# Performance work log

Measured on AMD Instinct MI355X. Metric: run time of the kernel, lower is better.

The kernel has to match this reference:

```python
import jax, jax.numpy as jnp
import numpy as np

NUM_HEADS = 32
NUM_KV_HEADS = 8
HEAD_DIM = 128
ROPE_THETA = 1000000.0
SCALING = HEAD_DIM ** -0.5


def apply_rope_neox(x, positions):
    # x: [T, H, D], positions: [T] int
    half = HEAD_DIM // 2
    inv_freq = 1.0 / (ROPE_THETA ** (jnp.arange(0, half, dtype=jnp.float32) / half))
    freqs = positions.astype(jnp.float32)[:, None] * inv_freq[None, :]  # [T, D/2]
    cos = jnp.cos(freqs)[:, None, :]  # [T, 1, D/2]
    sin = jnp.sin(freqs)[:, None, :]
    x1, x2 = x[..., :half], x[..., half:]
    return jnp.concatenate([x1 * cos - x2 * sin, x2 * cos + x1 * sin], axis=-1)


def setup_inputs() -> dict:
    key = jax.random.key(0)
    k1, k2, k3 = jax.random.split(key, 3)
    T, H = 2048, 4096
    positions = jnp.arange(T, dtype=jnp.int32)
    hidden_states = jax.random.normal(k1, (T, H), dtype=jnp.float32)
    Wqkv = jax.random.normal(k2, (H, 6144), dtype=jnp.float32) * 0.02
    Wo = jax.random.normal(k3, (H, H), dtype=jnp.float32) * 0.02
    return {"positions": positions, "hidden_states": hidden_states, "Wqkv": Wqkv, "Wo": Wo}


def reference(positions, hidden_states, Wqkv, Wo):
    T = hidden_states.shape[0]
    q_size = NUM_HEADS * HEAD_DIM
    kv_size = NUM_KV_HEADS * HEAD_DIM
    qkv = hidden_states @ Wqkv  # [T, 6144]
    q = qkv[:, :q_size].reshape(T, NUM_HEADS, HEAD_DIM)
    k = qkv[:, q_size:q_size + kv_size].reshape(T, NUM_KV_HEADS, HEAD_DIM)
    v = qkv[:, q_size + kv_size:].reshape(T, NUM_KV_HEADS, HEAD_DIM)
    q = apply_rope_neox(q, positions)
    k = apply_rope_neox(k, positions)
    # GQA: repeat kv heads to match query heads
    rep = NUM_HEADS // NUM_KV_HEADS
    k = jnp.repeat(k, rep, axis=1)  # [T, H, D]
    v = jnp.repeat(v, rep, axis=1)
    scores = jnp.einsum('thd,shd->hts', q, k) * SCALING  # [H, T, T]
    causal = jnp.tril(jnp.ones((T, T), dtype=bool))
    scores = jnp.where(causal[None], scores, jnp.finfo(scores.dtype).min)
    attn = jax.nn.softmax(scores, axis=-1)
    out = jnp.einsum('hts,shd->thd', attn, v).reshape(T, NUM_HEADS * HEAD_DIM)
    return out @ Wo
```

## Files before the change

kernel.cpp:

```cpp
#include <hip/hip_runtime.h>
#include <math.h>

#define T_TOK 2048
#define HDIM  4096
#define QKVN  6144
#define NHEADS 32
#define HD    128
#define KV_OFF 4096
#define V_OFF  5120
#define SCALE 0.08838834764831843f

typedef __attribute__((ext_vector_type(8))) short short8;
typedef __attribute__((ext_vector_type(4))) float f32x4;
typedef __attribute__((ext_vector_type(16))) float f32x16;

__device__ __forceinline__ ushort f2bf(float f) {
    union { float f; unsigned u; } v; v.f = f;
    unsigned r = v.u + 0x7FFFu + ((v.u >> 16) & 1u);
    return (ushort)(r >> 16);
}

template <int N_, int LDK, int KC>
__global__ __launch_bounds__(512, 2) void gemm_bf16_8ph(const ushort* __restrict__ A,
                                                        const ushort* __restrict__ B,
                                                        float* __restrict__ C0,
                                                        float* __restrict__ C1) {
    __shared__ __attribute__((aligned(16))) ushort As[2][2][8192];
    __shared__ __attribute__((aligned(16))) ushort Bs[2][2][8192];

    constexpr int NT = KC / 64;
    constexpr int NBN = N_ / 256;

    const int kz = blockIdx.y;
    float* __restrict__ C = kz ? C1 : C0;

    const int nwgx = (int)gridDim.x;
    const int bid = (int)blockIdx.x;
    const int swz = (nwgx & 7) ? bid : ((bid & 7) * (nwgx >> 3) + (bid >> 3));
    const int bm = (swz / NBN) * 256;
    const int bn = (swz % NBN) * 256;

    const int tid = (int)threadIdx.x;
    const int w = tid >> 6;
    const int l = tid & 63;
    const int hfa = w >> 2;
    const int hfb = (w & 3) >> 1;
    const int wbr64 = (w & 1) * 4096;

    const int arc = (l & 15) * 64;
    const int ac0 = ((((l >> 4) << 4)) ^ ((l & 7) << 4)) >> 1;
    const int ac1 = (((1 << 6) | ((l >> 4) << 4)) ^ ((l & 7) << 4)) >> 1;

    const int grow = w * 8 + (l >> 3);
    const int gcol = ((l & 7) ^ (l >> 3)) * 8;
    const ushort* Ag = A + (size_t)kz * KC + (size_t)(bm + grow) * LDK + gcol;
    const ushort* Bg = B + (size_t)kz * KC + (size_t)(bn + grow) * LDK + gcol;

    auto ldsA = (__attribute__((address_space(3))) char*)&As[0][0][0];
    auto ldsB = (__attribute__((address_space(3))) char*)&Bs[0][0][0];
    const int wsl = w * 1024;

#define STG2(ldsbase, gsrc, bufi, hfi, kt)                                                              \
    do {                                                                                                \
        __builtin_amdgcn_global_load_lds(                                                               \
            (const __attribute__((address_space(1))) void*)((gsrc) + (size_t)((hfi) * 128) * LDK + (kt) * 64),       \
            (__attribute__((address_space(3))) void*)((ldsbase) + (bufi) * 32768 + (hfi) * 16384 + wsl), 16, 0, 0);  \
        __builtin_amdgcn_global_load_lds(                                                               \
            (const __attribute__((address_space(1))) void*)((gsrc) + (size_t)((hfi) * 128 + 64) * LDK + (kt) * 64),  \
            (__attribute__((address_space(3))) void*)((ldsbase) + (bufi) * 32768 + (hfi) * 16384 + 8192 + wsl), 16, 0, 0); \
    } while (0)

    STG2(ldsB, Bg, 0, 0, 0);
    STG2(ldsB, Bg, 0, 1, 0);
    STG2(ldsA, Ag, 0, 0, 0);
    STG2(ldsA, Ag, 0, 1, 0);
    STG2(ldsB, Bg, 1, 0, 1);
    STG2(ldsB, Bg, 1, 1, 1);
    STG2(ldsA, Ag, 1, 0, 1);
    asm volatile("s_waitcnt vmcnt(6)" ::: "memory");
    __builtin_amdgcn_s_barrier();

    f32x4 acc[8][4];
#pragma unroll
    for (int i = 0; i < 8; i++)
#pragma unroll
        for (int j = 0; j < 4; j++) acc[i][j] = (f32x4){0.f, 0.f, 0.f, 0.f};

    short8 a0[4][2], a1[4][2], bq[4][2];

    int buf = 0;
    for (int t = 0; t < NT; ++t) {
        const int nb = buf ^ 1;
        const ushort* Abuf = &As[buf][hfa][0];
        const ushort* Bbuf = &Bs[buf][hfb][0] + wbr64;

#pragma unroll
        for (int fi = 0; fi < 4; fi++) {
            a0[fi][0] = *(const short8*)(Abuf + fi * 1024 + arc + ac0);
            a0[fi][1] = *(const short8*)(Abuf + fi * 1024 + arc + ac1);
        }
#pragma unroll
        for (int fj = 0; fj < 4; fj++) {
            bq[fj][0] = *(const short8*)(Bbuf + fj * 1024 + arc + ac0);
            bq[fj][1] = *(const short8*)(Bbuf + fj * 1024 + arc + ac1);
        }
        if (t + 1 < NT) STG2(ldsA, Ag, nb, 1, t + 1);
        __builtin_amdgcn_s_barrier();
        __builtin_amdgcn_s_setprio(1);
#pragma unroll
        for (int fi = 0; fi < 4; fi++)
#pragma unroll
            for (int fj = 0; fj < 2; fj++)
#pragma unroll
                for (int s = 0; s < 2; s++)
                    acc[fi][fj] = __builtin_amdgcn_mfma_f32_16x16x32_bf16(a0[fi][s], bq[fj][s], acc[fi][fj], 0, 0, 0);
        __builtin_amdgcn_s_setprio(0);
        __builtin_amdgcn_s_barrier();

        if (t + 2 < NT) STG2(ldsB, Bg, buf, 0, t + 2);
        __builtin_amdgcn_s_barrier();
        __builtin_amdgcn_s_setprio(1);
#pragma unroll
        for (int fi = 0; fi < 4; fi++)
#pragma unroll
            for (int fj = 2; fj < 4; fj++)
#pragma unroll
                for (int s = 0; s < 2; s++)
                    acc[fi][fj] = __builtin_amdgcn_mfma_f32_16x16x32_bf16(a0[fi][s], bq[fj][s], acc[fi][fj], 0, 0, 0);
        __builtin_amdgcn_s_setprio(0);
        __builtin_amdgcn_s_barrier();

#pragma unroll
        for (int fi = 0; fi < 4; fi++) {
            a1[fi][0] = *(const short8*)(Abuf + (fi + 4) * 1024 + arc + ac0);
            a1[fi][1] = *(const short8*)(Abuf + (fi + 4) * 1024 + arc + ac1);
        }
        if (t + 2 < NT) STG2(ldsB, Bg, buf, 1, t + 2);
        __builtin_amdgcn_s_barrier();
        __builtin_amdgcn_s_setprio(1);
#pragma unroll
        for (int fi = 0; fi < 4; fi++)
#pragma unroll
            for (int fj = 2; fj < 4; fj++)
#pragma unroll
                for (int s = 0; s < 2; s++)
                    acc[fi + 4][fj] = __builtin_amdgcn_mfma_f32_16x16x32_bf16(a1[fi][s], bq[fj][s], acc[fi + 4][fj], 0, 0, 0);
        __builtin_amdgcn_s_setprio(0);
        __builtin_amdgcn_s_barrier();

        if (t + 2 < NT) {
            STG2(ldsA, Ag, buf, 0, t + 2);
            asm volatile("s_waitcnt vmcnt(6)" ::: "memory");
        } else {
            asm volatile("s_waitcnt vmcnt(0)" ::: "memory");
        }
        __builtin_amdgcn_s_barrier();
        __builtin_amdgcn_s_setprio(1);
#pragma unroll
        for (int fi = 0; fi < 4; fi++)
#pragma unroll
            for (int fj = 0; fj < 2; fj++)
#pragma unroll
                for (int s = 0; s < 2; s++)
                    acc[fi + 4][fj] = __builtin_amdgcn_mfma_f32_16x16x32_bf16(a1[fi][s], bq[fj][s], acc[fi + 4][fj], 0, 0, 0);
        __builtin_amdgcn_s_setprio(0);
        __builtin_amdgcn_s_barrier();

        buf = nb;
    }
#undef STG2

    const int cn = bn + (w & 3) * 64 + (l & 15);
    const int rm = bm + hfa * 128 + ((l >> 4) << 2);
#pragma unroll
    for (int fi = 0; fi < 8; fi++)
#pragma unroll
        for (int fj = 0; fj < 4; fj++)
#pragma unroll
            for (int r = 0; r < 4; r++)
                C[(size_t)(rm + 16 * fi + r) * N_ + cn + 16 * fj] = acc[fi][fj][r];
}

__global__ __launch_bounds__(256) void add_f32(float* __restrict__ out,
                                               const float* __restrict__ p) {
    const int i = (blockIdx.x * 256 + threadIdx.x) * 4;
    float4 a = *(const float4*)(out + i);
    float4 b = *(const float4*)(p + i);
    a.x += b.x; a.y += b.y; a.z += b.z; a.w += b.w;
    *(float4*)(out + i) = a;
}

__global__ __launch_bounds__(256) void cast_bf16(const float* __restrict__ in,
                                                 ushort* __restrict__ outp) {
    const int i = (blockIdx.x * 256 + threadIdx.x) * 4;
    float4 v = *(const float4*)(in + i);
    ushort4 o = {f2bf(v.x), f2bf(v.y), f2bf(v.z), f2bf(v.w)};
    *(ushort4*)(outp + i) = o;
}

template <int K_, int N_>
__global__ __launch_bounds__(256) void transpose_cast(const float* __restrict__ W,
                                                      ushort* __restrict__ WT) {
    __shared__ float T[32 * 65];
    const int k0 = blockIdx.y * 32;
    const int n0 = blockIdx.x * 64;
    const int x = threadIdx.x & 63;
    const int y = threadIdx.x >> 6;
#pragma unroll
    for (int p = 0; p < 8; p++) {
        const int kk = p * 4 + y;
        T[kk * 65 + x] = W[(size_t)(k0 + kk) * N_ + n0 + x];
    }
    __syncthreads();
#pragma unroll
    for (int q = 0; q < 4; q++) {
        const int nl = q * 16 + (threadIdx.x >> 4);
        const int k2 = (threadIdx.x & 15) * 2;
        ushort2 o = {f2bf(T[k2 * 65 + nl]), f2bf(T[(k2 + 1) * 65 + nl])};
        *(ushort2*)&WT[(size_t)(n0 + nl) * K_ + k0 + k2] = o;
    }
}

__global__ __launch_bounds__(256) void rope_cast(const int* __restrict__ pos,
                                                 const float* __restrict__ qkv,
                                                 ushort* __restrict__ qkB) {
    const int t = blockIdx.x;
    const int slot = blockIdx.y * 4 + (threadIdx.x >> 6);
    const int d = threadIdx.x & 63;
    const float p = (float)pos[t];
    const float invf = exp2f(-(float)d * (19.931568569324174f / 64.0f));
    const float f = p * invf;
    const float c = cosf(f), s = sinf(f);
    const float sc = (slot < 32) ? SCALE : 1.0f;
    const float* base = qkv + (size_t)t * QKVN + slot * HD;
    ushort* ob = qkB + (size_t)t * QKVN + slot * HD;
    const float x1 = base[d];
    const float x2 = base[d + 64];
    ob[d]      = f2bf((x1 * c - x2 * s) * sc);
    ob[d + 64] = f2bf((x2 * c + x1 * s) * sc);
}

__global__ __launch_bounds__(256) void vt_cast(const float* __restrict__ qkv,
                                               ushort* __restrict__ Vt) {
    __shared__ float tile[32][33];
    const int t0 = blockIdx.x * 32;
    const int c0 = blockIdx.y * 32;
    const int tx = threadIdx.x & 31;
    const int ty = threadIdx.x >> 5;
#pragma unroll
    for (int i = 0; i < 4; i++) {
        const int tt = ty + 8 * i;
        tile[tt][tx] = qkv[(size_t)(t0 + tt) * QKVN + V_OFF + c0 + tx];
    }
    __syncthreads();
#pragma unroll
    for (int i = 0; i < 4; i++) {
        const int dd = ty + 8 * i;
        Vt[(size_t)(c0 + dd) * 2048 + t0 + tx] = f2bf(tile[tx][dd]);
    }
}

__global__ __launch_bounds__(256, 2) void flash_attn_mfma(
        const ushort* __restrict__ qkB,
        const ushort* __restrict__ Vt,
        ushort* __restrict__ attnB) {
    __shared__ ushort Kf[2][16 * 512];
    __shared__ ushort Vf[2][16 * 512];

    const int b = blockIdx.x;
    const int half = b >> 8;
    const int rest = b & 255;
    const int h = rest >> 3;
    const int q8 = rest & 7;
    const int qi = half ? (15 - q8) : q8;
    const int kvh = h >> 2;

    const int tid = threadIdx.x;
    const int w = tid >> 6;
    const int l = tid & 63;
    const int l31 = l & 31;
    const int hf = l >> 5;

    const int qg = qi * 128 + w * 32 + l31;

    short8 qf[8];
    {
        const ushort* qrow = qkB + (size_t)qg * QKVN + h * HD + hf * 8;
#pragma unroll
        for (int kt = 0; kt < 8; kt++)
            qf[kt] = *(const short8*)(qrow + kt * 16);
    }

    f32x16 O[4];
#pragma unroll
    for (int dt = 0; dt < 4; dt++)
#pragma unroll
        for (int r = 0; r < 16; r++) O[dt][r] = 0.f;
    float mcur = -INFINITY, lcur = 0.f;

    const ushort* kbase = qkB + (size_t)l31 * QKVN + KV_OFF + kvh * HD + (2 * w) * 16 + hf * 8;
    const ushort* vbase = Vt + ((size_t)(kvh * 128 + w * 32 + l31)) * 2048 + hf * 8;

    auto ldsK = (__attribute__((address_space(3))) char*)&Kf[0][0];
    auto ldsV = (__attribute__((address_space(3))) char*)&Vf[0][0];

    const int nst = 2 * qi + 2;
    const int mylast = (4 * qi + w) >> 1;

#define GLD(src, dst) __builtin_amdgcn_global_load_lds(                              \
        (const __attribute__((address_space(1))) void*)(src),                        \
        (__attribute__((address_space(3))) void*)(dst), 16, 0, 0)

#define AST64(j, bb)                                                                 \
    do {                                                                             \
        const ushort* kg0 = kbase + (size_t)(j) * 64 * QKVN;                         \
        const ushort* kg1 = kg0 + (size_t)32 * QKVN;                                 \
        GLD(kg0,      ldsK + (bb) * 16384 + (2 * w) * 1024);                         \
        GLD(kg0 + 16, ldsK + (bb) * 16384 + (2 * w + 1) * 1024);                     \
        GLD(kg1,      ldsK + (bb) * 16384 + (8 + 2 * w) * 1024);                     \
        GLD(kg1 + 16, ldsK + (bb) * 16384 + (8 + 2 * w + 1) * 1024);                 \
        const ushort* vg = vbase + (j) * 64;                                         \
        GLD(vg,       ldsV + (bb) * 16384 + (4 * w + 0) * 1024);                     \
        GLD(vg + 16,  ldsV + (bb) * 16384 + (4 * w + 1) * 1024);                     \
        GLD(vg + 32,  ldsV + (bb) * 16384 + (4 * w + 2) * 1024);                     \
        GLD(vg + 48,  ldsV + (bb) * 16384 + (4 * w + 3) * 1024);                     \
    } while (0)

    AST64(0, 0);

    for (int j = 0; j < nst; j++) {
        const int buf = j & 1;
        __builtin_amdgcn_s_barrier();
        if (j + 1 < nst) {
            AST64(j + 1, buf ^ 1);
            asm volatile("s_waitcnt vmcnt(8)" ::: "memory");
        } else {
            asm volatile("s_waitcnt vmcnt(0)" ::: "memory");
        }
        __builtin_amdgcn_s_barrier();

        if (j <= mylast) {
            const ushort* Kb = &Kf[buf][0];
            const ushort* Vb = &Vf[buf][0];
            f32x16 S0, S1;
#pragma unroll
            for (int r = 0; r < 16; r++) { S0[r] = 0.f; S1[r] = 0.f; }
            __builtin_amdgcn_s_setprio(1);
#pragma unroll
            for (int kt = 0; kt < 8; kt++) {
                short8 k0 = *(const short8*)(Kb + kt * 512 + l * 8);
                S0 = __builtin_amdgcn_mfma_f32_32x32x16_bf16(k0, qf[kt], S0, 0, 0, 0);
            }
#pragma unroll
            for (int kt = 0; kt < 8; kt++) {
                short8 k1 = *(const short8*)(Kb + (8 + kt) * 512 + l * 8);
                S1 = __builtin_amdgcn_mfma_f32_32x32x16_bf16(k1, qf[kt], S1, 0, 0, 0);
            }
            __builtin_amdgcn_s_setprio(0);

            if (j == mylast) {
                const int sb = j * 64 + 4 * hf;
#pragma unroll
                for (int r = 0; r < 16; r++) {
                    const int sg = sb + (r & 3) + 8 * (r >> 2);
                    if (sg > qg) S0[r] = -INFINITY;
                    if (sg + 32 > qg) S1[r] = -INFINITY;
                }
            }
            float rmax = S0[0];
#pragma unroll
            for (int r = 1; r < 16; r++) rmax = fmaxf(rmax, S0[r]);
#pragma unroll
            for (int r = 0; r < 16; r++) rmax = fmaxf(rmax, S1[r]);
            rmax = fmaxf(rmax, __shfl_xor(rmax, 32));
            const float mnew = fmaxf(mcur, rmax);
            const float alpha = __expf(mcur - mnew);
            float rsum = 0.f;
#pragma unroll
            for (int r = 0; r < 16; r++) {
                S0[r] = __expf(S0[r] - mnew);
                rsum += S0[r];
            }
#pragma unroll
            for (int r = 0; r < 16; r++) {
                S1[r] = __expf(S1[r] - mnew);
                rsum += S1[r];
            }
            rsum += __shfl_xor(rsum, 32);
            lcur = lcur * alpha + rsum;
            mcur = mnew;

#pragma unroll
            for (int dt = 0; dt < 4; dt++)
#pragma unroll
                for (int r = 0; r < 16; r++) O[dt][r] *= alpha;

            short8 Pf[4];
            {
                unsigned pk[8], rk[8];
#pragma unroll
                for (int g = 0; g < 4; g++) {
                    pk[2 * g]     = (unsigned)f2bf(S0[4 * g])     | ((unsigned)f2bf(S0[4 * g + 1]) << 16);
                    pk[2 * g + 1] = (unsigned)f2bf(S0[4 * g + 2]) | ((unsigned)f2bf(S0[4 * g + 3]) << 16);
                }
#pragma unroll
                for (int i = 0; i < 8; i++) rk[i] = (unsigned)__shfl_xor((int)pk[i], 32);
#pragma unroll
                for (int kt2 = 0; kt2 < 2; kt2++) {
                    const int g = 2 * kt2 + hf;
                    union { unsigned u[4]; short8 s; } cvt;
                    cvt.u[0] = hf ? rk[2 * g]     : pk[2 * g];
                    cvt.u[1] = hf ? rk[2 * g + 1] : pk[2 * g + 1];
                    cvt.u[2] = hf ? pk[2 * g]     : rk[2 * g];
                    cvt.u[3] = hf ? pk[2 * g + 1] : rk[2 * g + 1];
                    Pf[kt2] = cvt.s;
                }
#pragma unroll
                for (int g = 0; g < 4; g++) {
                    pk[2 * g]     = (unsigned)f2bf(S1[4 * g])     | ((unsigned)f2bf(S1[4 * g + 1]) << 16);
                    pk[2 * g + 1] = (unsigned)f2bf(S1[4 * g + 2]) | ((unsigned)f2bf(S1[4 * g + 3]) << 16);
                }
#pragma unroll
                for (int i = 0; i < 8; i++) rk[i] = (unsigned)__shfl_xor((int)pk[i], 32);
#pragma unroll
                for (int kt2 = 0; kt2 < 2; kt2++) {
                    const int g = 2 * kt2 + hf;
                    union { unsigned u[4]; short8 s; } cvt;
                    cvt.u[0] = hf ? rk[2 * g]     : pk[2 * g];
                    cvt.u[1] = hf ? rk[2 * g + 1] : pk[2 * g + 1];
                    cvt.u[2] = hf ? pk[2 * g]     : rk[2 * g];
                    cvt.u[3] = hf ? pk[2 * g + 1] : rk[2 * g + 1];
                    Pf[2 + kt2] = cvt.s;
                }
            }

            __builtin_amdgcn_s_setprio(1);
#pragma unroll
            for (int dt = 0; dt < 4; dt++)
#pragma unroll
                for (int ks = 0; ks < 4; ks++) {
                    short8 afV = *(const short8*)(Vb + (dt * 4 + ks) * 512 + l * 8);
                    O[dt] = __builtin_amdgcn_mfma_f32_32x32x16_bf16(afV, Pf[ks], O[dt], 0, 0, 0);
                }
            __builtin_amdgcn_s_setprio(0);
        }
    }
#undef AST64
#undef GLD

    const float inv = 1.0f / lcur;
    ushort* orow = attnB + (size_t)qg * HDIM + h * HD + 4 * hf;
#pragma unroll
    for (int dt = 0; dt < 4; dt++)
#pragma unroll
        for (int rg = 0; rg < 4; rg++) {
            ushort4 o;
            o.x = f2bf(O[dt][4 * rg + 0] * inv);
            o.y = f2bf(O[dt][4 * rg + 1] * inv);
            o.z = f2bf(O[dt][4 * rg + 2] * inv);
            o.w = f2bf(O[dt][4 * rg + 3] * inv);
            *(ushort4*)(orow + dt * 32 + 8 * rg) = o;
        }
}

__global__ __launch_bounds__(256) void rope_kernel(const int* __restrict__ pos,
                                                   float* __restrict__ qkv) {
    const int t = blockIdx.x;
    const int head = blockIdx.y * 4 + (threadIdx.x >> 6);
    const int d = threadIdx.x & 63;
    const float p = (float)pos[t];
    const float invf = exp2f(-(float)d * (19.931568569324174f / 64.0f));
    const float f = p * invf;
    const float c = cosf(f), s = sinf(f);
    float* base = qkv + (size_t)t * QKVN + head * HD;
    const float x1 = base[d];
    const float x2 = base[d + 64];
    base[d]      = x1 * c - x2 * s;
    base[d + 64] = x2 * c + x1 * s;
}

#define DOT4(acc, a, b) acc += (a).x*(b).x + (a).y*(b).y + (a).z*(b).z + (a).w*(b).w
#define FMA4(o, p, v) { (o).x += (p)*(v).x; (o).y += (p)*(v).y; (o).z += (p)*(v).z; (o).w += (p)*(v).w; }

__global__ __launch_bounds__(256, 2) void flash_attn_f32(const float* __restrict__ qkv,
                                                         float* __restrict__ out) {
    __shared__ float Qs[64 * 132];
    __shared__ float KVs[32 * 132];
    __shared__ float Ps[64 * 34];
    const int b = blockIdx.x;
    const int half = (b >> 9) & 1;
    const int rest = b & 511;
    const int h = rest >> 4;
    const int qlo = rest & 15;
    const int qi = half ? (31 - qlo) : qlo;
    const int kvh = h >> 2;
    const int tid = threadIdx.x;
    const int tx = tid & 7;
    const int ty = tid >> 3;
    {
        const float* qbase = qkv + (size_t)(qi * 64) * QKVN + h * HD;
#pragma unroll
        for (int r = 0; r < 8; r++) {
            int idx = r * 256 + tid;
            int qrow = idx >> 5;
            int d = (idx & 31) * 4;
            float4 v = *(const float4*)(qbase + (size_t)qrow * QKVN + d);
            v.x *= SCALE; v.y *= SCALE; v.z *= SCALE; v.w *= SCALE;
            *(float4*)(Qs + qrow * 132 + d) = v;
        }
    }
    float m[2], lsm[2];
    float4 O[2][4];
#pragma unroll
    for (int i = 0; i < 2; i++) {
        m[i] = -INFINITY; lsm[i] = 0.f;
#pragma unroll
        for (int jj = 0; jj < 4; jj++) O[i][jj] = make_float4(0.f, 0.f, 0.f, 0.f);
    }
    const float* kbase = qkv + KV_OFF + kvh * HD;
    const float* vbase = qkv + V_OFF + kvh * HD;
    const int qg0 = qi * 64 + ty;
    const int nst = 2 * qi + 2;
    for (int st = 0; st < nst; st++) {
        __syncthreads();
#pragma unroll
        for (int r = 0; r < 4; r++) {
            int idx = r * 256 + tid;
            int srow = idx >> 5;
            int d = (idx & 31) * 4;
            *(float4*)(KVs + srow * 132 + d) =
                *(const float4*)(kbase + (size_t)(st * 32 + srow) * QKVN + d);
        }
        __syncthreads();
        float S[2][4];
#pragma unroll
        for (int i = 0; i < 2; i++)
#pragma unroll
            for (int j = 0; j < 4; j++) S[i][j] = 0.f;
#pragma unroll 4
        for (int kk = 0; kk < HD; kk += 4) {
            float4 q0 = *(const float4*)(Qs + ty * 132 + kk);
            float4 q1 = *(const float4*)(Qs + (ty + 32) * 132 + kk);
            float4 k0 = *(const float4*)(KVs + tx * 132 + kk);
            float4 k1 = *(const float4*)(KVs + (tx + 8) * 132 + kk);
            float4 k2 = *(const float4*)(KVs + (tx + 16) * 132 + kk);
            float4 k3 = *(const float4*)(KVs + (tx + 24) * 132 + kk);
            DOT4(S[0][0], q0, k0); DOT4(S[0][1], q0, k1);
            DOT4(S[0][2], q0, k2); DOT4(S[0][3], q0, k3);
            DOT4(S[1][0], q1, k0); DOT4(S[1][1], q1, k1);
            DOT4(S[1][2], q1, k2); DOT4(S[1][3], q1, k3);
        }
        const int sg0 = st * 32 + tx;
        float alpha[2];
#pragma unroll
        for (int i = 0; i < 2; i++) {
            const int qg = qg0 + 32 * i;
            float rmax = -INFINITY;
#pragma unroll
            for (int j = 0; j < 4; j++) {
                if (sg0 + 8 * j > qg) S[i][j] = -INFINITY;
                rmax = fmaxf(rmax, S[i][j]);
            }
#pragma unroll
            for (int off = 1; off < 8; off <<= 1)
                rmax = fmaxf(rmax, __shfl_xor(rmax, off));
            const float mnew = fmaxf(m[i], rmax);
            alpha[i] = __expf(m[i] - mnew);
            float rsum = 0.f;
#pragma unroll
            for (int j = 0; j < 4; j++) {
                S[i][j] = __expf(S[i][j] - mnew);
                rsum += S[i][j];
            }
#pragma unroll
            for (int off = 1; off < 8; off <<= 1)
                rsum += __shfl_xor(rsum, off);
            lsm[i] = lsm[i] * alpha[i] + rsum;
            m[i] = mnew;
        }
#pragma unroll
        for (int i = 0; i < 2; i++)
#pragma unroll
            for (int j = 0; j < 4; j++)
                Ps[(ty + 32 * i) * 34 + tx + 8 * j] = S[i][j];
        __syncthreads();
#pragma unroll
        for (int r = 0; r < 4; r++) {
            int idx = r * 256 + tid;
            int srow = idx >> 5;
            int d = (idx & 31) * 4;
            *(float4*)(KVs + srow * 132 + d) =
                *(const float4*)(vbase + (size_t)(st * 32 + srow) * QKVN + d);
        }
        __syncthreads();
#pragma unroll
        for (int i = 0; i < 2; i++) {
            const float a = alpha[i];
#pragma unroll
            for (int jj = 0; jj < 4; jj++) {
                O[i][jj].x *= a; O[i][jj].y *= a; O[i][jj].z *= a; O[i][jj].w *= a;
            }
        }
#pragma unroll 4
        for (int s = 0; s < 32; s++) {
            float p0 = Ps[ty * 34 + s];
            float p1 = Ps[(ty + 32) * 34 + s];
            const float* vr = KVs + s * 132 + 4 * tx;
            float4 v0 = *(const float4*)(vr);
            float4 v1 = *(const float4*)(vr + 32);
            float4 v2 = *(const float4*)(vr + 64);
            float4 v3 = *(const float4*)(vr + 96);
            FMA4(O[0][0], p0, v0); FMA4(O[0][1], p0, v1);
            FMA4(O[0][2], p0, v2); FMA4(O[0][3], p0, v3);
            FMA4(O[1][0], p1, v0); FMA4(O[1][1], p1, v1);
            FMA4(O[1][2], p1, v2); FMA4(O[1][3], p1, v3);
        }
    }
#pragma unroll
    for (int i = 0; i < 2; i++) {
        const float inv = 1.0f / lsm[i];
        float* orow = out + (size_t)(qi * 64 + ty + 32 * i) * HDIM + h * HD + 4 * tx;
#pragma unroll
        for (int jj = 0; jj < 4; jj++) {
            float4 wv = O[i][jj];
            wv.x *= inv; wv.y *= inv; wv.z *= inv; wv.w *= inv;
            *(float4*)(orow + 32 * jj) = wv;
        }
    }
}

template <int N_, int K_>
__global__ __launch_bounds__(256) void sgemm(const float* __restrict__ A,
                                             const float* __restrict__ B,
                                             float* __restrict__ C) {
    __shared__ float As[8][128];
    __shared__ float Bs[8][128];
    const int tid = threadIdx.x;
    const int bm = blockIdx.y * 128;
    const int bn = blockIdx.x * 128;
    const int tx = tid & 15;
    const int ty = tid >> 4;
    const int lm = tid >> 1;
    const int lkq = (tid & 1) * 4;
    const int lr = tid >> 5;
    const int lnq = (tid & 31) * 4;
    float acc[8][8];
#pragma unroll
    for (int i = 0; i < 8; i++)
#pragma unroll
        for (int j = 0; j < 8; j++) acc[i][j] = 0.f;
    const float* Aptr = A + (size_t)(bm + lm) * K_ + lkq;
    const float* Bptr = B + (size_t)lr * N_ + bn + lnq;
    for (int k0 = 0; k0 < K_; k0 += 8) {
        float4 av = *(const float4*)Aptr;
        float4 bv = *(const float4*)Bptr;
        __syncthreads();
        As[lkq + 0][lm] = av.x;
        As[lkq + 1][lm] = av.y;
        As[lkq + 2][lm] = av.z;
        As[lkq + 3][lm] = av.w;
        *(float4*)&Bs[lr][lnq] = bv;
        __syncthreads();
        Aptr += 8;
        Bptr += (size_t)8 * N_;
#pragma unroll
        for (int kk = 0; kk < 8; kk++) {
            float4 a0 = *(const float4*)&As[kk][ty * 4];
            float4 a1 = *(const float4*)&As[kk][64 + ty * 4];
            float4 b0 = *(const float4*)&Bs[kk][tx * 4];
            float4 b1 = *(const float4*)&Bs[kk][64 + tx * 4];
            float a[8] = {a0.x, a0.y, a0.z, a0.w, a1.x, a1.y, a1.z, a1.w};
            float bb[8] = {b0.x, b0.y, b0.z, b0.w, b1.x, b1.y, b1.z, b1.w};
#pragma unroll
            for (int i = 0; i < 8; i++)
#pragma unroll
                for (int j = 0; j < 8; j++) acc[i][j] += a[i] * bb[j];
        }
    }
#pragma unroll
    for (int i = 0; i < 8; i++) {
        int row = bm + ((i < 4) ? (ty * 4 + i) : (64 + ty * 4 + i - 4));
        float4 c0 = {acc[i][0], acc[i][1], acc[i][2], acc[i][3]};
        float4 c1 = {acc[i][4], acc[i][5], acc[i][6], acc[i][7]};
        *(float4*)&C[(size_t)row * N_ + bn + tx * 4] = c0;
        *(float4*)&C[(size_t)row * N_ + bn + 64 + tx * 4] = c1;
    }
}

extern "C" void kernel_launch(void* const* d_in, const int* in_sizes, int n_in,
                              void* d_out, int out_size, void* d_ws, size_t ws_size,
                              hipStream_t stream) {
    const int*   positions = (const int*)d_in[0];
    const float* hidden    = (const float*)d_in[1];
    const float* Wqkv      = (const float*)d_in[2];
    const float* Wo        = (const float*)d_in[3];
    float* out = (float*)d_out;

    char* ws = (char*)d_ws;
    float*  qkv   = (float*)ws;
    ushort* attnB = (ushort*)ws;
    float*  Pk    = (float*)(ws + 16777216);
    ushort* WqkvT = (ushort*)(ws + 50331648);
    ushort* WoT   = (ushort*)(ws + 100663296);
    ushort* hA    = (ushort*)(ws + 134217728);
    ushort* qkB   = (ushort*)(ws + 134217728);
    ushort* Vt    = (ushort*)(ws + 159383552);
    const size_t NEEDED = 163577856;

    if (ws_size >= NEEDED) {
        cast_bf16<<<dim3((T_TOK * HDIM) / 1024), 256, 0, stream>>>(hidden, hA);
        transpose_cast<HDIM, QKVN><<<dim3(QKVN / 64, HDIM / 32), 256, 0, stream>>>(Wqkv, WqkvT);
        transpose_cast<HDIM, HDIM><<<dim3(HDIM / 64, HDIM / 32), 256, 0, stream>>>(Wo, WoT);
        gemm_bf16_8ph<QKVN, HDIM, HDIM>
            <<<dim3((T_TOK / 256) * (QKVN / 256), 1), 512, 0, stream>>>(hA, WqkvT, qkv, qkv);
        rope_cast<<<dim3(T_TOK, 10), 256, 0, stream>>>(positions, qkv, qkB);
        vt_cast<<<dim3(T_TOK / 32, 32), 256, 0, stream>>>(qkv, Vt);
        flash_attn_mfma<<<dim3(512), 256, 0, stream>>>(qkB, Vt, attnB);
        gemm_bf16_8ph<HDIM, HDIM, HDIM / 2>
            <<<dim3((T_TOK / 256) * (HDIM / 256), 2), 512, 0, stream>>>(attnB, WoT, out, Pk);
        add_f32<<<dim3((T_TOK * HDIM) / 1024), 256, 0, stream>>>(out, Pk);
    } else {
        float* attn = qkv + (size_t)T_TOK * QKVN;
        sgemm<QKVN, HDIM><<<dim3(QKVN / 128, T_TOK / 128), 256, 0, stream>>>(hidden, Wqkv, qkv);
        rope_kernel<<<dim3(T_TOK, 10), 256, 0, stream>>>(positions, qkv);
        flash_attn_f32<<<dim3(1024), 256, 0, stream>>>(qkv, attn);
        sgemm<HDIM, HDIM><<<dim3(HDIM / 128, T_TOK / 128), 256, 0, stream>>>(attn, Wo, out);
    }
}
```

Baseline: 616.3 us.

## Fuse RoPE and V-transpose casts into QKV GEMM epilogue; lazy softmax rescale

```diff
diff --git a/kernel.cpp b/kernel.cpp
--- a/kernel.cpp
+++ b/kernel.cpp
@@ -20,11 +20,14 @@
     return (ushort)(r >> 16);
 }
 
-template <int N_, int LDK, int KC>
+template <int N_, int LDK, int KC, int MODE>
 __global__ __launch_bounds__(512, 2) void gemm_bf16_8ph(const ushort* __restrict__ A,
                                                         const ushort* __restrict__ B,
                                                         float* __restrict__ C0,
-                                                        float* __restrict__ C1) {
+                                                        float* __restrict__ C1,
+                                                        const int* __restrict__ pos,
+                                                        ushort* __restrict__ qkB,
+                                                        ushort* __restrict__ Vt) {
     __shared__ __attribute__((aligned(16))) ushort As[2][2][8192];
     __shared__ __attribute__((aligned(16))) ushort Bs[2][2][8192];
 
@@ -32,7 +35,6 @@
     constexpr int NBN = N_ / 256;
 
     const int kz = blockIdx.y;
-    float* __restrict__ C = kz ? C1 : C0;
 
     const int nwgx = (int)gridDim.x;
     const int bid = (int)blockIdx.x;
@@ -170,15 +172,65 @@
     }
 #undef STG2
 
-    const int cn = bn + (w & 3) * 64 + (l & 15);
-    const int rm = bm + hfa * 128 + ((l >> 4) << 2);
-#pragma unroll
-    for (int fi = 0; fi < 8; fi++)
-#pragma unroll
-        for (int fj = 0; fj < 4; fj++)
-#pragma unroll
-            for (int r = 0; r < 4; r++)
-                C[(size_t)(rm + 16 * fi + r) * N_ + cn + 16 * fj] = acc[fi][fj][r];
+    if constexpr (MODE == 0) {
+        float* __restrict__ C = kz ? C1 : C0;
+        const int cn = bn + (w & 3) * 64 + (l & 15);
+        const int rm = bm + hfa * 128 + ((l >> 4) << 2);
+#pragma unroll
+        for (int fi = 0; fi < 8; fi++)
+#pragma unroll
+            for (int fj = 0; fj < 4; fj++)
+#pragma unroll
+                for (int r = 0; r < 4; r++)
+                    C[(size_t)(rm + 16 * fi + r) * N_ + cn + 16 * fj] = acc[fi][fj][r];
+    } else {
+        float* Ls = (float*)&As[0][0][0];
+        const bool isV = (bn >= V_OFF);
+        const int q = w & 3;
+        const int r4 = (l >> 4) << 2;
+#pragma unroll
+        for (int fi = 0; fi < 8; fi++) {
+#pragma unroll
+            for (int fj = 0; fj < 4; fj++)
+#pragma unroll
+                for (int r = 0; r < 4; r++)
+                    Ls[(hfa * 16 + r4 + r) * 260 + q * 64 + (l & 15) + 16 * fj] = acc[fi][fj][r];
+            __builtin_amdgcn_s_barrier();
+            if (!isV) {
+                const int trow = bm + hfa * 128 + 16 * fi + r4;
+#pragma unroll
+                for (int r = 0; r < 4; r++) {
+                    const int t = trow + r;
+                    const float p = (float)pos[t];
+#pragma unroll
+                    for (int fj = 0; fj < 4; fj++) {
+                        const int cr = q * 64 + (l & 15) + 16 * fj;
+                        const int dd = cr & 127;
+                        const int d64 = dd & 63;
+                        const float own = acc[fi][fj][r];
+                        const float prt = Ls[(hfa * 16 + r4 + r) * 260 + (cr ^ 64)];
+                        const float invf = exp2f(-(float)d64 * (19.931568569324174f / 64.0f));
+                        const float ang = p * invf;
+                        const float cf = __cosf(ang), sf = __sinf(ang);
+                        const float o = (dd < 64) ? (own * cf - prt * sf) : (own * cf + prt * sf);
+                        const float sc = (bn + cr < KV_OFF) ? SCALE : 1.0f;
+                        qkB[(size_t)t * QKVN + bn + cr] = f2bf(o * sc);
+                    }
+                }
+            } else {
+                const int vcr = tid >> 1;
+                const int hh = tid & 1;
+                union { ushort u[16]; short8 s[2]; } tmp;
+#pragma unroll
+                for (int rr = 0; rr < 16; rr++)
+                    tmp.u[rr] = f2bf(Ls[(hh * 16 + rr) * 260 + vcr]);
+                ushort* dst = Vt + (size_t)(bn - V_OFF + vcr) * 2048 + bm + hh * 128 + 16 * fi;
+                *(short8*)dst = tmp.s[0];
+                *(short8*)(dst + 8) = tmp.s[1];
+            }
+            __builtin_amdgcn_s_barrier();
+        }
+    }
 }
 
 __global__ __launch_bounds__(256) void add_f32(float* __restrict__ out,
@@ -218,45 +270,6 @@
         const int k2 = (threadIdx.x & 15) * 2;
         ushort2 o = {f2bf(T[k2 * 65 + nl]), f2bf(T[(k2 + 1) * 65 + nl])};
         *(ushort2*)&WT[(size_t)(n0 + nl) * K_ + k0 + k2] = o;
-    }
-}
-
-__global__ __launch_bounds__(256) void rope_cast(const int* __restrict__ pos,
-                                                 const float* __restrict__ qkv,
-                                                 ushort* __restrict__ qkB) {
-    const int t = blockIdx.x;
-    const int slot = blockIdx.y * 4 + (threadIdx.x >> 6);
-    const int d = threadIdx.x & 63;
-    const float p = (float)pos[t];
-    const float invf = exp2f(-(float)d * (19.931568569324174f / 64.0f));
-    const float f = p * invf;
-    const float c = cosf(f), s = sinf(f);
-    const float sc = (slot < 32) ? SCALE : 1.0f;
-    const float* base = qkv + (size_t)t * QKVN + slot * HD;
-    ushort* ob = qkB + (size_t)t * QKVN + slot * HD;
-    const float x1 = base[d];
-    const float x2 = base[d + 64];
-    ob[d]      = f2bf((x1 * c - x2 * s) * sc);
-    ob[d + 64] = f2bf((x2 * c + x1 * s) * sc);
-}
-
-__global__ __launch_bounds__(256) void vt_cast(const float* __restrict__ qkv,
-                                               ushort* __restrict__ Vt) {
-    __shared__ float tile[32][33];
-    const int t0 = blockIdx.x * 32;
-    const int c0 = blockIdx.y * 32;
-    const int tx = threadIdx.x & 31;
-    const int ty = threadIdx.x >> 5;
-#pragma unroll
-    for (int i = 0; i < 4; i++) {
-        const int tt = ty + 8 * i;
-        tile[tt][tx] = qkv[(size_t)(t0 + tt) * QKVN + V_OFF + c0 + tx];
-    }
-    __syncthreads();
-#pragma unroll
-    for (int i = 0; i < 4; i++) {
-        const int dd = ty + 8 * i;
-        Vt[(size_t)(c0 + dd) * 2048 + t0 + tx] = f2bf(tile[tx][dd]);
     }
 }
 
@@ -373,8 +386,12 @@
 #pragma unroll
             for (int r = 0; r < 16; r++) rmax = fmaxf(rmax, S1[r]);
             rmax = fmaxf(rmax, __shfl_xor(rmax, 32));
-            const float mnew = fmaxf(mcur, rmax);
-            const float alpha = __expf(mcur - mnew);
+
+            const unsigned long long need = __ballot(rmax > mcur + 8.0f);
+            float mnew, alpha;
+            if (need == 0) { mnew = mcur; alpha = 1.0f; }
+            else { mnew = fmaxf(mcur, rmax); alpha = __expf(mcur - mnew); }
+
             float rsum = 0.f;
 #pragma unroll
             for (int r = 0; r < 16; r++) {
@@ -390,10 +407,12 @@
             lcur = lcur * alpha + rsum;
             mcur = mnew;
 
-#pragma unroll
-            for (int dt = 0; dt < 4; dt++)
-#pragma unroll
-                for (int r = 0; r < 16; r++) O[dt][r] *= alpha;
+            if (need != 0) {
+#pragma unroll
+                for (int dt = 0; dt < 4; dt++)
+#pragma unroll
+                    for (int r = 0; r < 16; r++) O[dt][r] *= alpha;
+            }
 
             short8 Pf[4];
             {
@@ -697,29 +716,29 @@
     float* out = (float*)d_out;
 
     char* ws = (char*)d_ws;
-    float*  qkv   = (float*)ws;
-    ushort* attnB = (ushort*)ws;
-    float*  Pk    = (float*)(ws + 16777216);
+    ushort* qkB   = (ushort*)ws;
+    ushort* Vt    = (ushort*)(ws + 25165824);
+    ushort* attnB = (ushort*)(ws + 29360128);
+    float*  Pk    = (float*)(ws + 46137344);
     ushort* WqkvT = (ushort*)(ws + 50331648);
     ushort* WoT   = (ushort*)(ws + 100663296);
     ushort* hA    = (ushort*)(ws + 134217728);
-    ushort* qkB   = (ushort*)(ws + 134217728);
-    ushort* Vt    = (ushort*)(ws + 159383552);
     const size_t NEEDED = 163577856;
 
     if (ws_size >= NEEDED) {
         cast_bf16<<<dim3((T_TOK * HDIM) / 1024), 256, 0, stream>>>(hidden, hA);
         transpose_cast<HDIM, QKVN><<<dim3(QKVN / 64, HDIM / 32), 256, 0, stream>>>(Wqkv, WqkvT);
         transpose_cast<HDIM, HDIM><<<dim3(HDIM / 64, HDIM / 32), 256, 0, stream>>>(Wo, WoT);
-        gemm_bf16_8ph<QKVN, HDIM, HDIM>
-            <<<dim3((T_TOK / 256) * (QKVN / 256), 1), 512, 0, stream>>>(hA, WqkvT, qkv, qkv);
-        rope_cast<<<dim3(T_TOK, 10), 256, 0, stream>>>(positions, qkv, qkB);
-        vt_cast<<<dim3(T_TOK / 32, 32), 256, 0, stream>>>(qkv, Vt);
+        gemm_bf16_8ph<QKVN, HDIM, HDIM, 1>
+            <<<dim3((T_TOK / 256) * (QKVN / 256), 1), 512, 0, stream>>>(
+                hA, WqkvT, nullptr, nullptr, positions, qkB, Vt);
         flash_attn_mfma<<<dim3(512), 256, 0, stream>>>(qkB, Vt, attnB);
-        gemm_bf16_8ph<HDIM, HDIM, HDIM / 2>
-            <<<dim3((T_TOK / 256) * (HDIM / 256), 2), 512, 0, stream>>>(attnB, WoT, out, Pk);
+        gemm_bf16_8ph<HDIM, HDIM, HDIM / 2, 0>
+            <<<dim3((T_TOK / 256) * (HDIM / 256), 2), 512, 0, stream>>>(
+                attnB, WoT, out, Pk, nullptr, nullptr, nullptr);
         add_f32<<<dim3((T_TOK * HDIM) / 1024), 256, 0, stream>>>(out, Pk);
     } else {
+        float* qkv  = (float*)ws;
         float* attn = qkv + (size_t)T_TOK * QKVN;
         sgemm<QKVN, HDIM><<<dim3(QKVN / 128, T_TOK / 128), 256, 0, stream>>>(hidden, Wqkv, qkv);
         rope_kernel<<<dim3(T_TOK, 10), 256, 0, stream>>>(positions, qkv);
```

Result: faster. 604.2 us (-2.0%).
